# Optimization experiments

Hardware: AMD Instinct MI355X
Metric: run time of the kernel (lower is better)

Reference implementation:

```python
import jax, jax.numpy as jnp
import numpy as np

N, E = 50000, 800000
DIN, DOUT, DEDGE, HEADS = 128, 128, 64, 1


def setup_inputs() -> dict:
    key = jax.random.key(0)
    ks = jax.random.split(key, 16)
    s = 0.02
    inp = {
        "x": jax.random.normal(ks[0], (N, DIN), jnp.float32),
        "edge_index": jax.random.randint(ks[1], (2, E), 0, N, dtype=jnp.int32),
        "edge_attr": jax.random.normal(ks[2], (E, DEDGE), jnp.float32),
        # TransformerConv params (PyG defaults: q/k/v/skip have bias, lin_edge has no bias)
        "Wq": jax.random.normal(ks[3], (DIN, HEADS * DOUT), jnp.float32) * s,
        "bq": jnp.zeros((HEADS * DOUT,), jnp.float32),
        "Wk": jax.random.normal(ks[4], (DIN, HEADS * DOUT), jnp.float32) * s,
        "bk": jnp.zeros((HEADS * DOUT,), jnp.float32),
        "Wv": jax.random.normal(ks[5], (DIN, HEADS * DOUT), jnp.float32) * s,
        "bv": jnp.zeros((HEADS * DOUT,), jnp.float32),
        "We": jax.random.normal(ks[6], (DEDGE, HEADS * DOUT), jnp.float32) * s,
        "Wskip": jax.random.normal(ks[7], (DIN, HEADS * DOUT), jnp.float32) * s,
        "bskip": jnp.zeros((HEADS * DOUT,), jnp.float32),
        # LayerNorm
        "ln_g": jnp.ones((DOUT,), jnp.float32),
        "ln_b": jnp.zeros((DOUT,), jnp.float32),
        # GatedResidualConnection
        "Wres": jax.random.normal(ks[8], (DIN, DOUT), jnp.float32) * s,
        "bres": jnp.zeros((DOUT,), jnp.float32),
        "Wgate": jax.random.normal(ks[9], (DIN, 1), jnp.float32) * s,
        "bgate": jnp.zeros((1,), jnp.float32),
    }
    return inp


def _transformer_conv(x, edge_index, edge_attr, Wq, bq, Wk, bk, Wv, bv, We, Wskip, bskip):
    H, C = HEADS, DOUT
    src, dst = edge_index[0], edge_index[1]  # j -> i (aggregate at dst)
    q = (x @ Wq + bq).reshape(-1, H, C)
    k = (x @ Wk + bk).reshape(-1, H, C)
    v = (x @ Wv + bv).reshape(-1, H, C)
    e = (edge_attr @ We).reshape(-1, H, C)  # [E,H,C]
    k_j = k[src] + e
    v_j = v[src] + e
    q_i = q[dst]
    alpha = jnp.sum(q_i * k_j, axis=-1) / jnp.sqrt(jnp.float32(C))  # [E,H]
    # segment softmax over incoming edges of each dst node
    amax = jax.ops.segment_max(alpha, dst, num_segments=N)  # [N,H]
    ex = jnp.exp(alpha - amax[dst])
    denom = jax.ops.segment_sum(ex, dst, num_segments=N)  # [N,H]
    p = ex / denom[dst]  # [E,H]
    out = jax.ops.segment_sum(p[..., None] * v_j, dst, num_segments=N)  # [N,H,C]
    out = out.reshape(-1, H * C)
    out = out + (x @ Wskip + bskip)  # root weight skip
    return out


def reference(x, edge_index, edge_attr, Wq, bq, Wk, bk, Wv, bv, We, Wskip, bskip,
              ln_g, ln_b, Wres, bres, Wgate, bgate):
    out = _transformer_conv(x, edge_index, edge_attr, Wq, bq, Wk, bk, Wv, bv, We, Wskip, bskip)
    # LayerNorm(out_channels)
    mu = jnp.mean(out, axis=-1, keepdims=True)
    var = jnp.mean(jnp.square(out - mu), axis=-1, keepdims=True)
    out = (out - mu) / jnp.sqrt(var + 1e-5) * ln_g + ln_b
    out = jax.nn.relu(out)
    # gated residual
    residual = x @ Wres + bres
    gate = jax.nn.sigmoid(x @ Wgate + bgate)  # [N,1]
    return gate * out + (1.0 - gate) * residual
```

## Files before the change

### kernel.cpp

```cpp
#include <hip/hip_runtime.h>
#include <math.h>

#define NN 50000
#define EE 800000
#define NPAD 50048
#define PC 768

typedef short bf16x8 __attribute__((ext_vector_type(8)));
typedef float f32x4 __attribute__((ext_vector_type(4)));

#define ASCALE 0.08838834764831845f

__device__ inline unsigned short f2bf(float f)
{
    unsigned u = __float_as_uint(f);
    u = u + 0x7fff + ((u >> 16) & 1);
    return (unsigned short)(u >> 16);
}

__device__ inline float bfu(unsigned short us)
{
    return __uint_as_float((unsigned)us << 16);
}

#define NXB (NPAD * 128 / 4 / 256)
__global__ __launch_bounds__(256) void k_prep(const float* __restrict__ x,
                                              short* __restrict__ Xb,
                                              const float* __restrict__ Wq,
                                              const float* __restrict__ bq,
                                              const float* __restrict__ We,
                                              float* __restrict__ wqe,
                                              float* __restrict__ bqe)
{
    if (blockIdx.x < NXB) {
        int t = blockIdx.x * 256 + threadIdx.x;
        int base = t * 4;
        short s0 = 0, s1 = 0, s2 = 0, s3 = 0;
        if (base < NN * 128) {
            const float4 v = *(const float4*)(x + base);
            s0 = f2bf(v.x); s1 = f2bf(v.y); s2 = f2bf(v.z); s3 = f2bf(v.w);
        }
        short4 o; o.x = s0; o.y = s1; o.z = s2; o.w = s3;
        *(short4*)(Xb + base) = o;
    } else {
        int idx = (blockIdx.x - NXB) * 256 + threadIdx.x;
        if (idx < 8192) {
            int r = idx >> 6, m = idx & 63;
            float acc = 0.f;
            for (int c = 0; c < 128; ++c) acc += Wq[r * 128 + c] * We[m * 128 + c];
            wqe[r * 64 + m] = acc;
        } else if (idx < 8256) {
            int m = idx - 8192;
            float acc = 0.f;
            for (int c = 0; c < 128; ++c) acc += bq[c] * We[m * 128 + c];
            bqe[m] = acc;
        }
    }
}

__global__ __launch_bounds__(256) void k_packw(
    const float* __restrict__ Wq, const float* __restrict__ bq,
    const float* __restrict__ Wk, const float* __restrict__ bk,
    const float* __restrict__ Wv, const float* __restrict__ bv,
    const float* __restrict__ Wskip, const float* __restrict__ bskip,
    const float* __restrict__ Wres, const float* __restrict__ bres,
    const float* __restrict__ Wgate, const float* __restrict__ bgate,
    const float* __restrict__ wqe, const float* __restrict__ bqe,
    const float* __restrict__ We,
    short* __restrict__ WT, float* __restrict__ bias,
    unsigned short* __restrict__ WeTb)
{
    int idx = blockIdx.x * 256 + threadIdx.x;
    if (idx < PC * 128) {
        int col = idx >> 7, k = idx & 127;
        float v;
        if (col < 128)      v = Wq[k * 128 + col];
        else if (col < 384) {
            int t = col - 128, c = t >> 2, s = t & 3;
            v = (s == 0) ? Wk[k * 128 + c] : (s == 1) ? Wk[k * 128 + c + 64]
              : (s == 2) ? Wv[k * 128 + c] : Wv[k * 128 + c + 64];
        }
        else if (col < 512) v = Wskip[k * 128 + (col - 384)];
        else if (col < 640) v = Wres[k * 128 + (col - 512)];
        else if (col < 704) v = wqe[k * 64 + (col - 640)];
        else if (col == 704) v = Wgate[k];
        else                v = 0.f;
        WT[col * 128 + k] = (short)f2bf(v);
    } else if (idx < PC * 128 + PC) {
        int col = idx - PC * 128;
        float b;
        if (col < 128)      b = bq[col];
        else if (col < 384) {
            int t = col - 128, c = t >> 2, s = t & 3;
            b = (s == 0) ? bk[c] : (s == 1) ? bk[c + 64]
              : (s == 2) ? bv[c] : bv[c + 64];
        }
        else if (col < 512) b = bskip[col - 384];
        else if (col < 640) b = bres[col - 512];
        else if (col < 704) b = bqe[col - 640];
        else if (col == 704) b = bgate[0];
        else                b = 0.f;
        bias[col] = b;
    } else if (idx < PC * 128 + PC + 128 * 72) {
        int i2 = idx - (PC * 128 + PC);
        int c = i2 / 72, kk = i2 % 72;
        WeTb[i2] = (kk < 64) ? f2bf(We[kk * 128 + c]) : (unsigned short)0;
    }
}

#define LROW 136
__global__ __launch_bounds__(256) void k_gemm(const short* __restrict__ Xb,
                                              const short* __restrict__ WT,
                                              const float* __restrict__ bias,
                                              float* __restrict__ Pq,
                                              unsigned short* __restrict__ Pe,
                                              unsigned short* __restrict__ KVb16)
{
    __shared__ short Al[128 * LROW];
    __shared__ short Bl[64 * LROW];

    int bn = blockIdx.x;
    int bm = blockIdx.y;
    int tid = threadIdx.x;

    const short* gA = Xb + (size_t)bm * 128 * 128;
    const short* gB = WT + (size_t)bn * 64 * 128;

#pragma unroll
    for (int it = 0; it < 8; ++it) {
        int g = it * 256 + tid;
        int row = g >> 4, c8 = g & 15;
        *(bf16x8*)&Al[row * LROW + c8 * 8] = *(const bf16x8*)(gA + g * 8);
    }
#pragma unroll
    for (int it = 0; it < 4; ++it) {
        int g = it * 256 + tid;
        int row = g >> 4, c8 = g & 15;
        *(bf16x8*)&Bl[row * LROW + c8 * 8] = *(const bf16x8*)(gB + g * 8);
    }
    __syncthreads();

    int wave = tid >> 6, lane = tid & 63;
    int quad = lane >> 4, l16 = lane & 15;
    int r0 = wave * 32;

    f32x4 acc[2][4] = {};
#pragma unroll
    for (int ks = 0; ks < 4; ++ks) {
        int k0 = ks * 32 + quad * 8;
        bf16x8 af0 = *(const bf16x8*)&Al[(r0 + l16) * LROW + k0];
        bf16x8 af1 = *(const bf16x8*)&Al[(r0 + 16 + l16) * LROW + k0];
#pragma unroll
        for (int cn = 0; cn < 4; ++cn) {
            bf16x8 bfr = *(const bf16x8*)&Bl[(cn * 16 + l16) * LROW + k0];
            acc[0][cn] = __builtin_amdgcn_mfma_f32_16x16x32_bf16(bfr, af0, acc[0][cn], 0, 0, 0);
            acc[1][cn] = __builtin_amdgcn_mfma_f32_16x16x32_bf16(bfr, af1, acc[1][cn], 0, 0, 0);
        }
    }

    bool isKV = (bn >= 2 && bn <= 5);
#pragma unroll
    for (int half = 0; half < 2; ++half) {
        int grow = bm * 128 + r0 + half * 16 + l16;
        if (grow < NN) {
#pragma unroll
            for (int cn = 0; cn < 4; ++cn) {
                int colbase = bn * 64 + cn * 16 + quad * 4;
                const float4 b4 = *(const float4*)(bias + colbase);
                float v0 = acc[half][cn][0] + b4.x;
                float v1 = acc[half][cn][1] + b4.y;
                float v2 = acc[half][cn][2] + b4.z;
                float v3 = acc[half][cn][3] + b4.w;
                if (bn < 2) {
                    float4 o; o.x = v0; o.y = v1; o.z = v2; o.w = v3;
                    *(float4*)(Pq + (size_t)grow * 128 + colbase) = o;
                } else if (isKV) {
                    uint2 o;
                    o.x = (unsigned)f2bf(v0) | ((unsigned)f2bf(v1) << 16);
                    o.y = (unsigned)f2bf(v2) | ((unsigned)f2bf(v3) << 16);
                    *(uint2*)(KVb16 + (size_t)grow * 256 + (colbase - 128)) = o;
                } else {
                    if (colbase == 704) v0 = 1.f / (1.f + __expf(-v0));
                    uint2 o;
                    o.x = (unsigned)f2bf(v0) | ((unsigned)f2bf(v1) << 16);
                    o.y = (unsigned)f2bf(v2) | ((unsigned)f2bf(v3) << 16);
                    *(uint2*)(Pe + (size_t)grow * 384 + (colbase - 384)) = o;
                }
            }
        }
    }
}

__global__ __launch_bounds__(256) void k_hist(const int* __restrict__ ei,
                                              int* __restrict__ deg, int E)
{
    int e = blockIdx.x * 256 + threadIdx.x;
    if (e < E) atomicAdd(&deg[ei[E + e]], 1);
}

__global__ __launch_bounds__(256) void k_scan1(const int* __restrict__ deg,
                                               int* __restrict__ rs,
                                               int* __restrict__ cs, int n)
{
    __shared__ int sh[256];
    int base = blockIdx.x * 1024;
    int t = threadIdx.x;
    int idx = base + t * 4;
    int v[4];
#pragma unroll
    for (int k = 0; k < 4; ++k) v[k] = (idx + k < n) ? deg[idx + k] : 0;
    int sum = v[0] + v[1] + v[2] + v[3];
    sh[t] = sum;
    __syncthreads();
    for (int off = 1; off < 256; off <<= 1) {
        int add = (t >= off) ? sh[t - off] : 0;
        __syncthreads();
        sh[t] += add;
        __syncthreads();
    }
    int run = sh[t] - sum;
    if (t == 255) cs[blockIdx.x] = sh[255];
#pragma unroll
    for (int k = 0; k < 4; ++k) {
        if (idx + k < n) rs[idx + k] = run;
        run += v[k];
    }
}

__global__ void k_scan2(int* __restrict__ cs, int nc)
{
    __shared__ int sh[64];
    int t = threadIdx.x;
    sh[t] = (t < nc) ? cs[t] : 0;
    __syncthreads();
    if (t == 0) {
        int acc = 0;
        for (int i = 0; i < nc; ++i) { int v = sh[i]; sh[i] = acc; acc += v; }
    }
    __syncthreads();
    if (t < nc) cs[t] = sh[t];
}

__global__ __launch_bounds__(256) void k_scan3(int* __restrict__ rs,
                                               const int* __restrict__ cs,
                                               int* __restrict__ cur, int n, int E)
{
    int i = blockIdx.x * 256 + threadIdx.x;
    if (i < n) {
        int v = rs[i] + cs[i >> 10];
        rs[i] = v;
        cur[i] = v;
    } else if (i == n) {
        rs[n] = E;
    }
}

__global__ __launch_bounds__(256) void k_scatter(const int* __restrict__ ei,
                                                 int* __restrict__ cur,
                                                 int2* __restrict__ sj, int E)
{
    int e = blockIdx.x * 256 + threadIdx.x;
    if (e < E) {
        int d = ei[E + e];
        int pos = atomicAdd(&cur[d], 1);
        int2 v; v.x = ei[e]; v.y = e;
        sj[pos] = v;
    }
}

__global__ __launch_bounds__(256) void k_attn_fused(
    const float* __restrict__ Pq, const unsigned short* __restrict__ Pe,
    const unsigned int* __restrict__ KVb,
    const float* __restrict__ ea, const unsigned short* __restrict__ WeTb,
    const int* __restrict__ rs, const int2* __restrict__ sj,
    const float* __restrict__ ln_g, const float* __restrict__ ln_b,
    float* __restrict__ out)
{
    __shared__ unsigned short Sb_l[4 * 64];
    __shared__ float att_l[4 * 128];

    int tid = threadIdx.x;
    int wave = tid >> 6, lane = tid & 63;
    int node = blockIdx.x * 4 + wave;

    const float* Qrow = Pq + (size_t)node * 128;
    const unsigned short* Erow = Pe + (size_t)node * 384;
    float q0 = Qrow[lane];
    float q1 = Qrow[64 + lane];
    float wq = bfu(Erow[256 + lane]);

    float accd = 0.f, t0 = 0.f, t1 = 0.f, sA = 0.f;
    int beg = rs[node], end = rs[node + 1];

    int p = beg;
    for (; p + 8 <= end; p += 8) {
        float pp[8], aa[8], v0[8], v1[8];
#pragma unroll
        for (int u = 0; u < 8; ++u) {
            long long sv = __builtin_nontemporal_load((const long long*)(sj + p + u));
            int sx = (int)sv, sy = (int)(sv >> 32);
            uint2 kv2 = *(const uint2*)(KVb + (size_t)sx * 128 + 2 * lane);
            float a = __builtin_nontemporal_load(ea + (size_t)sy * 64 + lane);
            float k0 = __uint_as_float(kv2.x << 16);
            float k1 = __uint_as_float(kv2.x & 0xffff0000u);
            v0[u] = __uint_as_float(kv2.y << 16);
            v1[u] = __uint_as_float(kv2.y & 0xffff0000u);
            aa[u] = a;
            pp[u] = q0 * k0 + q1 * k1 + wq * a;
        }
#pragma unroll
        for (int o = 32; o > 0; o >>= 1) {
#pragma unroll
            for (int u = 0; u < 8; ++u) pp[u] += __shfl_xor(pp[u], o);
        }
#pragma unroll
        for (int u = 0; u < 8; ++u) {
            float ex = __expf(pp[u] * ASCALE);
            accd += ex;
            t0 += ex * v0[u];
            t1 += ex * v1[u];
            sA += ex * aa[u];
        }
    }
    for (; p + 4 <= end; p += 4) {
        float pp[4], aa[4], v0[4], v1[4];
#pragma unroll
        for (int u = 0; u < 4; ++u) {
            long long sv = __builtin_nontemporal_load((const long long*)(sj + p + u));
            int sx = (int)sv, sy = (int)(sv >> 32);
            uint2 kv2 = *(const uint2*)(KVb + (size_t)sx * 128 + 2 * lane);
            float a = __builtin_nontemporal_load(ea + (size_t)sy * 64 + lane);
            float k0 = __uint_as_float(kv2.x << 16);
            float k1 = __uint_as_float(kv2.x & 0xffff0000u);
            v0[u] = __uint_as_float(kv2.y << 16);
            v1[u] = __uint_as_float(kv2.y & 0xffff0000u);
            aa[u] = a;
            pp[u] = q0 * k0 + q1 * k1 + wq * a;
        }
#pragma unroll
        for (int o = 32; o > 0; o >>= 1) {
#pragma unroll
            for (int u = 0; u < 4; ++u) pp[u] += __shfl_xor(pp[u], o);
        }
#pragma unroll
        for (int u = 0; u < 4; ++u) {
            float ex = __expf(pp[u] * ASCALE);
            accd += ex;
            t0 += ex * v0[u];
            t1 += ex * v1[u];
            sA += ex * aa[u];
        }
    }
    for (; p < end; ++p) {
        long long sv = __builtin_nontemporal_load((const long long*)(sj + p));
        int sx = (int)sv, sy = (int)(sv >> 32);
        uint2 kv2 = *(const uint2*)(KVb + (size_t)sx * 128 + 2 * lane);
        float a = __builtin_nontemporal_load(ea + (size_t)sy * 64 + lane);
        float k0 = __uint_as_float(kv2.x << 16);
        float k1 = __uint_as_float(kv2.x & 0xffff0000u);
        float vv0 = __uint_as_float(kv2.y << 16);
        float vv1 = __uint_as_float(kv2.y & 0xffff0000u);
        float part = q0 * k0 + q1 * k1 + wq * a;
#pragma unroll
        for (int o = 32; o > 0; o >>= 1) part += __shfl_xor(part, o);
        float ex = __expf(part * ASCALE);
        accd += ex;
        t0 += ex * vv0;
        t1 += ex * vv1;
        sA += ex * a;
    }


    Sb_l[wave * 64 + lane] = f2bf(sA);
    __syncthreads();

    {
        int quad = lane >> 4, l16 = lane & 15;
        int arow = l16 & 3;
        bf16x8 a0 = *(const bf16x8*)&Sb_l[arow * 64 + quad * 8];
        bf16x8 a1 = *(const bf16x8*)&Sb_l[arow * 64 + 32 + quad * 8];
#pragma unroll
        for (int c2 = 0; c2 < 2; ++c2) {
            int cn = wave * 2 + c2;
            int r = cn * 16 + l16;
            bf16x8 b0 = *(const bf16x8*)(WeTb + r * 72 + quad * 8);
            bf16x8 b1 = *(const bf16x8*)(WeTb + r * 72 + 32 + quad * 8);
            f32x4 acc = {};
            acc = __builtin_amdgcn_mfma_f32_16x16x32_bf16(a0, b0, acc, 0, 0, 0);
            acc = __builtin_amdgcn_mfma_f32_16x16x32_bf16(a1, b1, acc, 0, 0, 0);
            if (quad == 0) {
#pragma unroll
                for (int i = 0; i < 4; ++i)
                    att_l[i * 128 + cn * 16 + l16] = acc[i];
            }
        }
    }
    __syncthreads();

    float rcp = accd > 0.f ? 1.f / accd : 0.f;
    float a0f = (t0 + att_l[wave * 128 + lane]) * rcp + bfu(Erow[lane]);
    float a1f = (t1 + att_l[wave * 128 + 64 + lane]) * rcp + bfu(Erow[64 + lane]);

    float s = a0f + a1f;
#pragma unroll
    for (int o = 32; o > 0; o >>= 1) s += __shfl_xor(s, o);
    float mean = s * (1.f / 128.f);
    float d0 = a0f - mean, d1 = a1f - mean;
    float vs = d0 * d0 + d1 * d1;
#pragma unroll
    for (int o = 32; o > 0; o >>= 1) vs += __shfl_xor(vs, o);
    float inv = rsqrtf(vs * (1.f / 128.f) + 1e-5f);
    float n0 = d0 * inv * ln_g[lane] + ln_b[lane];
    float n1 = d1 * inv * ln_g[64 + lane] + ln_b[64 + lane];
    n0 = fmaxf(n0, 0.f);
    n1 = fmaxf(n1, 0.f);

    float g = bfu(Erow[320]);
    float r0 = bfu(Erow[128 + lane]);
    float r1 = bfu(Erow[192 + lane]);
    out[(size_t)node * 128 + lane] = g * n0 + (1.f - g) * r0;
    out[(size_t)node * 128 + 64 + lane] = g * n1 + (1.f - g) * r1;
}

extern "C" void kernel_launch(void* const* d_in, const int* in_sizes, int n_in,
                              void* d_out, int out_size, void* d_ws, size_t ws_size,
                              hipStream_t stream)
{
    const float* x     = (const float*)d_in[0];
    const int*   ei    = (const int*)d_in[1];
    const float* ea    = (const float*)d_in[2];
    const float* Wq    = (const float*)d_in[3];
    const float* bq    = (const float*)d_in[4];
    const float* Wk    = (const float*)d_in[5];
    const float* bk    = (const float*)d_in[6];
    const float* Wv    = (const float*)d_in[7];
    const float* bv    = (const float*)d_in[8];
    const float* We    = (const float*)d_in[9];
    const float* Wskip = (const float*)d_in[10];
    const float* bskip = (const float*)d_in[11];
    const float* ln_g  = (const float*)d_in[12];
    const float* ln_b  = (const float*)d_in[13];
    const float* Wres  = (const float*)d_in[14];
    const float* bres  = (const float*)d_in[15];
    const float* Wgate = (const float*)d_in[16];
    const float* bgate = (const float*)d_in[17];
    float* out = (float*)d_out;

    float* W = (float*)d_ws;
    size_t o = 0;
    auto falloc = [&](size_t e) { size_t r = o; o += e; return r; };
    size_t oPQ   = falloc((size_t)NN * 128);
    size_t oWQE  = falloc(8192);
    size_t oBQE  = falloc(64);
    size_t oBIAS = falloc(PC);
    size_t oKVB  = falloc((size_t)NN * 128);

    short* SB = (short*)(W + o);
    size_t oXB  = 0;
    size_t oWT  = oXB + (size_t)NPAD * 128;
    size_t oWET = oWT + (size_t)PC * 128;
    size_t oPE  = oWET + 128 * 72;
    size_t sh_total = oPE + (size_t)NN * 384;

    int* IB = (int*)(SB + ((sh_total + 1) & ~(size_t)1));
    size_t io = 0;
    auto ialloc = [&](size_t e) { size_t r = io; io += e; return r; };
    size_t oSJ   = ialloc((size_t)2 * EE);
    size_t oDEG  = ialloc(NN);
    size_t oRS   = ialloc(NN + 1);
    size_t oCUR  = ialloc(NN);
    size_t oCS   = ialloc(64);

    hipMemsetAsync(IB + oDEG, 0, NN * sizeof(int), stream);

    k_prep<<<NXB + 33, 256, 0, stream>>>(x, SB + oXB, Wq, bq, We,
                                         W + oWQE, W + oBQE);
    k_packw<<<(PC * 128 + PC + 128 * 72 + 255) / 256, 256, 0, stream>>>(
        Wq, bq, Wk, bk, Wv, bv, Wskip, bskip, Wres, bres, Wgate, bgate,
        W + oWQE, W + oBQE, We, SB + oWT, W + oBIAS,
        (unsigned short*)(SB + oWET));

    dim3 ggrid(PC / 64, NPAD / 128);
    k_gemm<<<ggrid, 256, 0, stream>>>(SB + oXB, SB + oWT, W + oBIAS, W + oPQ,
                                      (unsigned short*)(SB + oPE),
                                      (unsigned short*)(W + oKVB));

    k_hist<<<(EE + 255) / 256, 256, 0, stream>>>(ei, IB + oDEG, EE);
    k_scan1<<<49, 256, 0, stream>>>(IB + oDEG, IB + oRS, IB + oCS, NN);
    k_scan2<<<1, 64, 0, stream>>>(IB + oCS, 49);
    k_scan3<<<(NN + 256) / 256, 256, 0, stream>>>(IB + oRS, IB + oCS, IB + oCUR, NN, EE);
    k_scatter<<<(EE + 255) / 256, 256, 0, stream>>>(ei, IB + oCUR, (int2*)(IB + oSJ), EE);

    k_attn_fused<<<NN / 4, 256, 0, stream>>>(
        W + oPQ, (const unsigned short*)(SB + oPE),
        (const unsigned int*)(W + oKVB), ea,
        (const unsigned short*)(SB + oWET),
        IB + oRS, (const int2*)(IB + oSJ), ln_g, ln_b, out);
}
```

Before: 547.7 us.

## Merge prep, weight packing and degree histogram into one launch; fuse scan stages

Combines the x-to-bf16 conversion, weight packing (now computing the Wq·We product inline), and the destination-degree histogram into one kernel launch. The two-level scan's second stage moves into the first via an atomic ticket, so the last block does the block-sum prefix. The GEMM also drops its LDS staging of B and reads weight fragments straight from global memory. The goal is fewer launches and serialisation points. The risks are redundant inline dot products in packing and uncoalesced global B reads inside the MFMA loop.

Result: slower. 584.8 us (+6.8%).

```diff
diff --git a/kernel.cpp b/kernel.cpp
--- a/kernel.cpp
+++ b/kernel.cpp
@@ -24,16 +24,24 @@
 }
 
 #define NXB (NPAD * 128 / 4 / 256)
-__global__ __launch_bounds__(256) void k_prep(const float* __restrict__ x,
-                                              short* __restrict__ Xb,
-                                              const float* __restrict__ Wq,
-                                              const float* __restrict__ bq,
-                                              const float* __restrict__ We,
-                                              float* __restrict__ wqe,
-                                              float* __restrict__ bqe)
-{
-    if (blockIdx.x < NXB) {
-        int t = blockIdx.x * 256 + threadIdx.x;
+#define PWB 423
+#define HB  ((EE + 255) / 256)
+__global__ __launch_bounds__(256) void k_front(
+    const float* __restrict__ x, short* __restrict__ Xb,
+    const float* __restrict__ Wq, const float* __restrict__ bq,
+    const float* __restrict__ Wk, const float* __restrict__ bk,
+    const float* __restrict__ Wv, const float* __restrict__ bv,
+    const float* __restrict__ We,
+    const float* __restrict__ Wskip, const float* __restrict__ bskip,
+    const float* __restrict__ Wres, const float* __restrict__ bres,
+    const float* __restrict__ Wgate, const float* __restrict__ bgate,
+    short* __restrict__ WT, float* __restrict__ bias,
+    unsigned short* __restrict__ WeTb,
+    const int* __restrict__ ei, int* __restrict__ deg)
+{
+    int b = blockIdx.x;
+    if (b < NXB) {
+        int t = b * 256 + threadIdx.x;
         int base = t * 4;
         short s0 = 0, s1 = 0, s2 = 0, s3 = 0;
         if (base < NN * 128) {
@@ -42,69 +50,56 @@
         }
         short4 o; o.x = s0; o.y = s1; o.z = s2; o.w = s3;
         *(short4*)(Xb + base) = o;
+    } else if (b < NXB + PWB) {
+        int idx = (b - NXB) * 256 + threadIdx.x;
+        if (idx < PC * 128) {
+            int col = idx >> 7, k = idx & 127;
+            float v;
+            if (col < 128)      v = Wq[k * 128 + col];
+            else if (col < 384) {
+                int t2 = col - 128, c = t2 >> 2, s = t2 & 3;
+                v = (s == 0) ? Wk[k * 128 + c] : (s == 1) ? Wk[k * 128 + c + 64]
+                  : (s == 2) ? Wv[k * 128 + c] : Wv[k * 128 + c + 64];
+            }
+            else if (col < 512) v = Wskip[k * 128 + (col - 384)];
+            else if (col < 640) v = Wres[k * 128 + (col - 512)];
+            else if (col < 704) {
+                int m = col - 640;
+                float acc = 0.f;
+                for (int c = 0; c < 128; ++c) acc += Wq[k * 128 + c] * We[m * 128 + c];
+                v = acc;
+            }
+            else if (col == 704) v = Wgate[k];
+            else                v = 0.f;
+            WT[col * 128 + k] = (short)f2bf(v);
+        } else if (idx < PC * 128 + PC) {
+            int col = idx - PC * 128;
+            float bb;
+            if (col < 128)      bb = bq[col];
+            else if (col < 384) {
+                int t2 = col - 128, c = t2 >> 2, s = t2 & 3;
+                bb = (s == 0) ? bk[c] : (s == 1) ? bk[c + 64]
+                   : (s == 2) ? bv[c] : bv[c + 64];
+            }
+            else if (col < 512) bb = bskip[col - 384];
+            else if (col < 640) bb = bres[col - 512];
+            else if (col < 704) {
+                int m = col - 640;
+                float acc = 0.f;
+                for (int c = 0; c < 128; ++c) acc += bq[c] * We[m * 128 + c];
+                bb = acc;
+            }
+            else if (col == 704) bb = bgate[0];
+            else                bb = 0.f;
+            bias[col] = bb;
+        } else if (idx < PC * 128 + PC + 128 * 72) {
+            int i2 = idx - (PC * 128 + PC);
+            int c = i2 / 72, kk = i2 % 72;
+            WeTb[i2] = (kk < 64) ? f2bf(We[kk * 128 + c]) : (unsigned short)0;
+        }
     } else {
-        int idx = (blockIdx.x - NXB) * 256 + threadIdx.x;
-        if (idx < 8192) {
-            int r = idx >> 6, m = idx & 63;
-            float acc = 0.f;
-            for (int c = 0; c < 128; ++c) acc += Wq[r * 128 + c] * We[m * 128 + c];
-            wqe[r * 64 + m] = acc;
-        } else if (idx < 8256) {
-            int m = idx - 8192;
-            float acc = 0.f;
-            for (int c = 0; c < 128; ++c) acc += bq[c] * We[m * 128 + c];
-            bqe[m] = acc;
-        }
-    }
-}
-
-__global__ __launch_bounds__(256) void k_packw(
-    const float* __restrict__ Wq, const float* __restrict__ bq,
-    const float* __restrict__ Wk, const float* __restrict__ bk,
-    const float* __restrict__ Wv, const float* __restrict__ bv,
-    const float* __restrict__ Wskip, const float* __restrict__ bskip,
-    const float* __restrict__ Wres, const float* __restrict__ bres,
-    const float* __restrict__ Wgate, const float* __restrict__ bgate,
-    const float* __restrict__ wqe, const float* __restrict__ bqe,
-    const float* __restrict__ We,
-    short* __restrict__ WT, float* __restrict__ bias,
-    unsigned short* __restrict__ WeTb)
-{
-    int idx = blockIdx.x * 256 + threadIdx.x;
-    if (idx < PC * 128) {
-        int col = idx >> 7, k = idx & 127;
-        float v;
-        if (col < 128)      v = Wq[k * 128 + col];
-        else if (col < 384) {
-            int t = col - 128, c = t >> 2, s = t & 3;
-            v = (s == 0) ? Wk[k * 128 + c] : (s == 1) ? Wk[k * 128 + c + 64]
-              : (s == 2) ? Wv[k * 128 + c] : Wv[k * 128 + c + 64];
-        }
-        else if (col < 512) v = Wskip[k * 128 + (col - 384)];
-        else if (col < 640) v = Wres[k * 128 + (col - 512)];
-        else if (col < 704) v = wqe[k * 64 + (col - 640)];
-        else if (col == 704) v = Wgate[k];
-        else                v = 0.f;
-        WT[col * 128 + k] = (short)f2bf(v);
-    } else if (idx < PC * 128 + PC) {
-        int col = idx - PC * 128;
-        float b;
-        if (col < 128)      b = bq[col];
-        else if (col < 384) {
-            int t = col - 128, c = t >> 2, s = t & 3;
-            b = (s == 0) ? bk[c] : (s == 1) ? bk[c + 64]
-              : (s == 2) ? bv[c] : bv[c + 64];
-        }
-        else if (col < 512) b = bskip[col - 384];
-        else if (col < 640) b = bres[col - 512];
-        else if (col < 704) b = bqe[col - 640];
-        else if (col == 704) b = bgate[0];
-        else                b = 0.f;
-        bias[col] = b;
-    } else if (idx < PC * 128 + PC + 128 * 72) {
-        int i2 = idx - (PC * 128 + PC);
-        int c = i2 / 72, kk = i2 % 72;
-        WeTb[i2] = (kk < 64) ? f2bf(We[kk * 128 + c]) : (unsigned short)0;
+        int e = (b - NXB - PWB) * 256 + threadIdx.x;
+        if (e < EE) atomicAdd(&deg[ei[EE + e]], 1);
     }
 }
 
@@ -117,7 +112,6 @@
                                               unsigned short* __restrict__ KVb16)
 {
     __shared__ short Al[128 * LROW];
-    __shared__ short Bl[64 * LROW];
 
     int bn = blockIdx.x;
     int bm = blockIdx.y;
@@ -132,12 +126,6 @@
         int row = g >> 4, c8 = g & 15;
         *(bf16x8*)&Al[row * LROW + c8 * 8] = *(const bf16x8*)(gA + g * 8);
     }
-#pragma unroll
-    for (int it = 0; it < 4; ++it) {
-        int g = it * 256 + tid;
-        int row = g >> 4, c8 = g & 15;
-        *(bf16x8*)&Bl[row * LROW + c8 * 8] = *(const bf16x8*)(gB + g * 8);
-    }
     __syncthreads();
 
     int wave = tid >> 6, lane = tid & 63;
@@ -152,7 +140,7 @@
         bf16x8 af1 = *(const bf16x8*)&Al[(r0 + 16 + l16) * LROW + k0];
 #pragma unroll
         for (int cn = 0; cn < 4; ++cn) {
-            bf16x8 bfr = *(const bf16x8*)&Bl[(cn * 16 + l16) * LROW + k0];
+            bf16x8 bfr = *(const bf16x8*)(gB + (cn * 16 + l16) * 128 + k0);
             acc[0][cn] = __builtin_amdgcn_mfma_f32_16x16x32_bf16(bfr, af0, acc[0][cn], 0, 0, 0);
             acc[1][cn] = __builtin_amdgcn_mfma_f32_16x16x32_bf16(bfr, af1, acc[1][cn], 0, 0, 0);
         }
@@ -191,16 +179,10 @@
     }
 }
 
-__global__ __launch_bounds__(256) void k_hist(const int* __restrict__ ei,
-                                              int* __restrict__ deg, int E)
-{
-    int e = blockIdx.x * 256 + threadIdx.x;
-    if (e < E) atomicAdd(&deg[ei[E + e]], 1);
-}
-
-__global__ __launch_bounds__(256) void k_scan1(const int* __restrict__ deg,
-                                               int* __restrict__ rs,
-                                               int* __restrict__ cs, int n)
+__global__ __launch_bounds__(256) void k_scan12(const int* __restrict__ deg,
+                                                int* __restrict__ rs,
+                                                int* __restrict__ cs,
+                                                int* __restrict__ ticket, int n)
 {
     __shared__ int sh[256];
     int base = blockIdx.x * 1024;
@@ -225,20 +207,15 @@
         if (idx + k < n) rs[idx + k] = run;
         run += v[k];
     }
-}
-
-__global__ void k_scan2(int* __restrict__ cs, int nc)
-{
-    __shared__ int sh[64];
-    int t = threadIdx.x;
-    sh[t] = (t < nc) ? cs[t] : 0;
-    __syncthreads();
+    __threadfence();
     if (t == 0) {
-        int acc = 0;
-        for (int i = 0; i < nc; ++i) { int v = sh[i]; sh[i] = acc; acc += v; }
-    }
-    __syncthreads();
-    if (t < nc) cs[t] = sh[t];
+        int tk = atomicAdd(ticket, 1);
+        if (tk == 48) {
+            __threadfence();
+            int acc = 0;
+            for (int i = 0; i < 49; ++i) { int vv = cs[i]; cs[i] = acc; acc += vv; }
+        }
+    }
 }
 
 __global__ __launch_bounds__(256) void k_scan3(int* __restrict__ rs,
@@ -450,8 +427,6 @@
     size_t o = 0;
     auto falloc = [&](size_t e) { size_t r = o; o += e; return r; };
     size_t oPQ   = falloc((size_t)NN * 128);
-    size_t oWQE  = falloc(8192);
-    size_t oBQE  = falloc(64);
     size_t oBIAS = falloc(PC);
     size_t oKVB  = falloc((size_t)NN * 128);
 
@@ -467,27 +442,25 @@
     auto ialloc = [&](size_t e) { size_t r = io; io += e; return r; };
     size_t oSJ   = ialloc((size_t)2 * EE);
     size_t oDEG  = ialloc(NN);
+    size_t oTK   = ialloc(1);
     size_t oRS   = ialloc(NN + 1);
     size_t oCUR  = ialloc(NN);
     size_t oCS   = ialloc(64);
 
-    hipMemsetAsync(IB + oDEG, 0, NN * sizeof(int), stream);
-
-    k_prep<<<NXB + 33, 256, 0, stream>>>(x, SB + oXB, Wq, bq, We,
-                                         W + oWQE, W + oBQE);
-    k_packw<<<(PC * 128 + PC + 128 * 72 + 255) / 256, 256, 0, stream>>>(
-        Wq, bq, Wk, bk, Wv, bv, Wskip, bskip, Wres, bres, Wgate, bgate,
-        W + oWQE, W + oBQE, We, SB + oWT, W + oBIAS,
-        (unsigned short*)(SB + oWET));
+    hipMemsetAsync(IB + oDEG, 0, (NN + 1) * sizeof(int), stream);
+
+    k_front<<<NXB + PWB + HB, 256, 0, stream>>>(
+        x, SB + oXB, Wq, bq, Wk, bk, Wv, bv, We,
+        Wskip, bskip, Wres, bres, Wgate, bgate,
+        SB + oWT, W + oBIAS, (unsigned short*)(SB + oWET),
+        ei, IB + oDEG);
 
     dim3 ggrid(PC / 64, NPAD / 128);
     k_gemm<<<ggrid, 256, 0, stream>>>(SB + oXB, SB + oWT, W + oBIAS, W + oPQ,
                                       (unsigned short*)(SB + oPE),
                                       (unsigned short*)(W + oKVB));
 
-    k_hist<<<(EE + 255) / 256, 256, 0, stream>>>(ei, IB + oDEG, EE);
-    k_scan1<<<49, 256, 0, stream>>>(IB + oDEG, IB + oRS, IB + oCS, NN);
-    k_scan2<<<1, 64, 0, stream>>>(IB + oCS, 49);
+    k_scan12<<<49, 256, 0, stream>>>(IB + oDEG, IB + oRS, IB + oCS, IB + oTK, NN);
     k_scan3<<<(NN + 256) / 256, 256, 0, stream>>>(IB + oRS, IB + oCS, IB + oCUR, NN, EE);
     k_scatter<<<(EE + 255) / 256, 256, 0, stream>>>(ei, IB + oCUR, (int2*)(IB + oSJ), EE);
 
```
